# Optimization experiments

Hardware: AMD Instinct MI355X
Metric: run time of the kernel (lower is better)

The kernel has to match this reference:

```python
import jax, jax.numpy as jnp
import numpy as np

SIGNAL_DIM = 64   # D
STATE_DIM = 64    # N
SEQ_LEN = 16384   # L
BATCH = 16


def _init_dplr_hippo(state_dim):
    """NumPy port of init_DPLR_HiPPO(signal_dim=1, state_dim). Returns Lambda,(N,) P,(N,) B,(N,1) complex64."""
    n = np.arange(state_dim, dtype=np.float64)
    A = np.zeros((state_dim, state_dim))
    for k in range(state_dim):
        A[k:, k] = np.sqrt(2.0 * np.arange(k, state_dim) + 1.0) * np.sqrt(2.0 * k + 1.0)
        A[k, k] = k + 1
    A = -A
    P = np.sqrt(n + 0.5)
    SI = A + P[:, None] * P[None, :]
    diag = np.diagonal(SI).copy()
    S = SI - np.diag(diag)
    eigvals, V = np.linalg.eigh(S * -1j)   # S*-1j is Hermitian
    Lam = diag + 1j * eigvals
    Vc = V.conj().T
    Pc = Vc @ P.astype(np.complex128)
    B = np.sqrt(2.0 * n + 1.0)[:, None]    # (N, 1): signal_dim=1, tied across channels
    Bc = Vc @ B.astype(np.complex128)
    return Lam.astype(np.complex64), Pc.astype(np.complex64), Bc.astype(np.complex64)


def _ri(x):
    # complex -> (..., 2) float32, matching torch.view_as_real parameter storage
    return jnp.stack([jnp.real(x), jnp.imag(x)], axis=-1).astype(jnp.float32)


def _to_c(x):
    return jax.lax.complex(x[..., 0], x[..., 1])


def setup_inputs() -> dict:
    key = jax.random.key(0)
    ku, kc1, kc2, kd, ks = jax.random.split(key, 5)
    Lam, P, B = _init_dplr_hippo(STATE_DIM)
    C = (jax.random.normal(kc1, (SIGNAL_DIM, STATE_DIM)) +
         1j * jax.random.normal(kc2, (SIGNAL_DIM, STATE_DIM))).astype(jnp.complex64)
    return {
        "u": jax.random.normal(ku, (BATCH, SEQ_LEN, SIGNAL_DIM), dtype=jnp.float32),
        "Lambda_ri": _ri(jnp.asarray(Lam)),      # (N, 2)
        "P_ri": _ri(jnp.asarray(P)),             # (N, 2)
        "B_ri": _ri(jnp.asarray(B)),             # (N, 1, 2)
        "C_ri": _ri(C),                          # (D, N, 2)
        "D_param": jax.random.normal(kd, (SIGNAL_DIM,), dtype=jnp.float32),
        "log_step": jnp.log(jax.random.uniform(ks, (1,), minval=0.001, maxval=0.1)).astype(jnp.float32),
    }


def reference(u, Lambda_ri, P_ri, B_ri, C_ri, D_param, log_step):
    Lam = _to_c(Lambda_ri)   # (N,)
    P = _to_c(P_ri)          # (N,)
    B = _to_c(B_ri)          # (N, 1)
    C = _to_c(C_ri)          # (D, N)
    L = u.shape[-2]

    step = jnp.exp(log_step)                                  # (1,)
    Omega = jnp.exp(-2j * jnp.pi * (jnp.arange(L) / L))       # (L,) roots of unity
    g = (2.0 / step) * ((1.0 - Omega) / (1.0 + Omega))        # (L,)

    # Batched Cauchy kernel: k_ab[l] = sum_n a_n * b_n / (g_l - Lambda_n)
    cauchy = 1.0 / (g[:, None] - Lam[None, :])                # (L, N)
    a0 = jnp.conj(C)        # (D, N)
    a1 = jnp.conj(P)        # (N,)
    b0 = B[:, 0]            # (N,)  == B.T row (signal_dim=1)
    b1 = P                  # (N,)
    k00 = jnp.einsum('dn,n,ln->dl', a0, b0, cauchy)
    k01 = jnp.einsum('dn,n,ln->dl', a0, b1, cauchy)
    k10 = jnp.einsum('n,n,ln->l', a1, b0, cauchy)
    k11 = jnp.einsum('n,n,ln->l', a1, b1, cauchy)

    evaluated = (2.0 / (1.0 + Omega)) * (k00 - k01 * (1.0 / (1.0 + k11)) * k10)  # (D, L)
    K = jnp.fft.ifft(evaluated, axis=-1).T.real               # (L, D) conv kernel

    # FFT convolution along time axis (zero-pad to 2L, linear convolution)
    ud = jnp.fft.rfft(jnp.pad(u, ((0, 0), (0, L), (0, 0))), axis=-2)
    Kd = jnp.fft.rfft(jnp.pad(K, ((0, L), (0, 0))), axis=-2)
    y = jnp.fft.irfft(ud * Kd, n=2 * L, axis=-2)[..., :L, :]
    return y + D_param * u
```

## Files before the change

kernel.cpp:

```cpp
#include <hip/hip_runtime.h>
#include <math.h>

#define MF 16384
#define HALF 8192

__device__ __forceinline__ float2 cmul(float2 a, float2 b){ return make_float2(a.x*b.x - a.y*b.y, a.x*b.y + a.y*b.x); }
__device__ __forceinline__ float2 cmulc(float2 a, float2 b){ return make_float2(a.x*b.x + a.y*b.y, a.y*b.x - a.x*b.y); }
__device__ __forceinline__ int rho4(int v){ return ((v & 3) << 2) | (v >> 2); }
__device__ __forceinline__ int sob(int k){
    return (rho4(k & 15) << 10) | (rho4((k >> 4) & 15) << 6) | (rho4((k >> 8) & 15) << 2) | (k >> 12);
}
__device__ __forceinline__ int ph(int e){ return e ^ ((e >> 4) & 3) ^ (((e >> 6) & 3) << 2); }

__device__ __forceinline__ void bf4f(float2&a,float2&b,float2&c,float2&d){
    float t0x=a.x+c.x, t0y=a.y+c.y, t2x=a.x-c.x, t2y=a.y-c.y;
    float t1x=b.x+d.x, t1y=b.y+d.y, t3x=b.x-d.x, t3y=b.y-d.y;
    a=make_float2(t0x+t1x,t0y+t1y);
    b=make_float2(t2x+t3y,t2y-t3x);
    c=make_float2(t0x-t1x,t0y-t1y);
    d=make_float2(t2x-t3y,t2y+t3x);
}
__device__ __forceinline__ void bf4i(float2&a,float2&b,float2&c,float2&d){
    float t0x=a.x+c.x, t0y=a.y+c.y, t2x=a.x-c.x, t2y=a.y-c.y;
    float t1x=b.x+d.x, t1y=b.y+d.y, t3x=b.x-d.x, t3y=b.y-d.y;
    a=make_float2(t0x+t1x,t0y+t1y);
    b=make_float2(t2x-t3y,t2y+t3x);
    c=make_float2(t0x-t1x,t0y-t1y);
    d=make_float2(t2x+t3y,t2y-t3x);
}

#define W16_1 make_float2(0.92387953251128674f, -0.38268343236508978f)
#define W16_2 make_float2(0.70710678118654752f, -0.70710678118654752f)
#define W16_3 make_float2(0.38268343236508978f, -0.92387953251128674f)
#define W16_6 make_float2(-0.70710678118654752f, -0.70710678118654752f)
#define W16_9 make_float2(-0.92387953251128674f, 0.38268343236508978f)

__device__ __forceinline__ void dft16_fwd(float2* x){
    bf4f(x[0],x[4],x[8],x[12]);
    bf4f(x[1],x[5],x[9],x[13]);
    bf4f(x[2],x[6],x[10],x[14]);
    bf4f(x[3],x[7],x[11],x[15]);
    x[5]=cmul(x[5],W16_1);  x[9]=cmul(x[9],W16_2);   x[13]=cmul(x[13],W16_3);
    x[6]=cmul(x[6],W16_2);  { float2 t=x[10]; x[10]=make_float2(t.y,-t.x); } x[14]=cmul(x[14],W16_6);
    x[7]=cmul(x[7],W16_3);  x[11]=cmul(x[11],W16_6); x[15]=cmul(x[15],W16_9);
    bf4f(x[0],x[1],x[2],x[3]);
    bf4f(x[4],x[5],x[6],x[7]);
    bf4f(x[8],x[9],x[10],x[11]);
    bf4f(x[12],x[13],x[14],x[15]);
}
__device__ __forceinline__ void dft16_inv(float2* x){
    bf4i(x[0],x[1],x[2],x[3]);
    bf4i(x[4],x[5],x[6],x[7]);
    bf4i(x[8],x[9],x[10],x[11]);
    bf4i(x[12],x[13],x[14],x[15]);
    x[5]=cmulc(x[5],W16_1); x[9]=cmulc(x[9],W16_2);  x[13]=cmulc(x[13],W16_3);
    x[6]=cmulc(x[6],W16_2); { float2 t=x[10]; x[10]=make_float2(-t.y,t.x); } x[14]=cmulc(x[14],W16_6);
    x[7]=cmulc(x[7],W16_3); x[11]=cmulc(x[11],W16_6); x[15]=cmulc(x[15],W16_9);
    bf4i(x[0],x[4],x[8],x[12]);
    bf4i(x[1],x[5],x[9],x[13]);
    bf4i(x[2],x[6],x[10],x[14]);
    bf4i(x[3],x[7],x[11],x[15]);
}

template<bool INV>
__device__ __forceinline__ void pass0(float2* A, const float2* bas, int tid){
    float2 x[16];
    int base = ph(tid);
    #pragma unroll
    for(int m=0;m<16;++m) x[m] = A[base + (m<<10)];
    float2 w1 = bas[tid];
    float2 w2=cmul(w1,w1), w4=cmul(w2,w2), w8=cmul(w4,w4);
    float2 w3=cmul(w2,w1), w5=cmul(w4,w1), w6=cmul(w4,w2), w7=cmul(w4,w3);
    float2 w9=cmul(w8,w1), w10=cmul(w8,w2), w11=cmul(w8,w3), w12=cmul(w8,w4);
    float2 w13=cmul(w8,w5), w14=cmul(w8,w6), w15=cmul(w8,w7);
    if (!INV){
        dft16_fwd(x);
        x[1]=cmul(x[1],w4);   x[2]=cmul(x[2],w8);   x[3]=cmul(x[3],w12);
        x[4]=cmul(x[4],w1);   x[5]=cmul(x[5],w5);   x[6]=cmul(x[6],w9);
        x[7]=cmul(x[7],w13);  x[8]=cmul(x[8],w2);   x[9]=cmul(x[9],w6);
        x[10]=cmul(x[10],w10);x[11]=cmul(x[11],w14);x[12]=cmul(x[12],w3);
        x[13]=cmul(x[13],w7); x[14]=cmul(x[14],w11);x[15]=cmul(x[15],w15);
    } else {
        x[1]=cmulc(x[1],w4);   x[2]=cmulc(x[2],w8);   x[3]=cmulc(x[3],w12);
        x[4]=cmulc(x[4],w1);   x[5]=cmulc(x[5],w5);   x[6]=cmulc(x[6],w9);
        x[7]=cmulc(x[7],w13);  x[8]=cmulc(x[8],w2);   x[9]=cmulc(x[9],w6);
        x[10]=cmulc(x[10],w10);x[11]=cmulc(x[11],w14);x[12]=cmulc(x[12],w3);
        x[13]=cmulc(x[13],w7); x[14]=cmulc(x[14],w11);x[15]=cmulc(x[15],w15);
        dft16_inv(x);
    }
    #pragma unroll
    for(int m=0;m<16;++m) A[base + (m<<10)] = x[m];
}

template<bool INV>
__device__ __forceinline__ void pass1(float2* A, const float2* tw1s, int tid){
    float2 x[16];
    int i1 = tid & 63;
    int B = (tid >> 6) << 10;
    int i1x = i1 ^ ((i1 >> 4) & 3);
    #pragma unroll
    for(int m=0;m<16;++m) x[m] = A[B + (m<<6) + (i1x ^ ((m&3)<<2))];
    if (!INV){
        dft16_fwd(x);
        #pragma unroll
        for(int j=1;j<16;++j) x[j] = cmul(x[j], tw1s[(j<<6)+i1]);
    } else {
        #pragma unroll
        for(int j=1;j<16;++j) x[j] = cmulc(x[j], tw1s[(j<<6)+i1]);
        dft16_inv(x);
    }
    #pragma unroll
    for(int m=0;m<16;++m) A[B + (m<<6) + (i1x ^ ((m&3)<<2))] = x[m];
}

template<bool INV>
__device__ __forceinline__ void pass2(float2* A, const float2* tw2s, int tid){
    float2 x[16];
    int q = tid >> 2, j2 = tid & 3;
    int qb = q << 6;
    int qx = (q & 3) << 2;
    #pragma unroll
    for(int m=0;m<16;++m) x[m] = A[qb + ((((m<<2)|j2) ^ ((m>>2)&3)) ^ qx)];
    if (!INV){
        dft16_fwd(x);
        #pragma unroll
        for(int j=1;j<16;++j) x[j] = cmul(x[j], tw2s[(j<<2)+j2]);
    } else {
        #pragma unroll
        for(int j=1;j<16;++j) x[j] = cmulc(x[j], tw2s[(j<<2)+j2]);
        dft16_inv(x);
    }
    #pragma unroll
    for(int m=0;m<16;++m) A[qb + ((((m<<2)|j2) ^ ((m>>2)&3)) ^ qx)] = x[m];
}

template<bool INV>
__device__ __forceinline__ void pass3(float2* A, int tid){
    int sgm = ((tid>>2)&3) ^ (((tid>>4)&3)<<2);
    #pragma unroll
    for(int rr=0; rr<4; ++rr){
        int base = (tid<<2) | (rr<<12);
        float2 a=A[(base|0)^sgm], b=A[(base|1)^sgm], c=A[(base|2)^sgm], d=A[(base|3)^sgm];
        if(!INV) bf4f(a,b,c,d); else bf4i(a,b,c,d);
        A[(base|0)^sgm]=a; A[(base|1)^sgm]=b; A[(base|2)^sgm]=c; A[(base|3)^sgm]=d;
    }
}

__global__ void k_init(float2* __restrict__ baseg, float2* __restrict__ tw1g, float2* __restrict__ tw2g){
    int id = blockIdx.x * 256 + threadIdx.x;
    const double TP = 6.2831853071795864769;
    if (id < 1024){
        double a = -TP * (double)id / 16384.0;
        baseg[id] = make_float2((float)cos(a), (float)sin(a));
    } else if (id < 2048){
        int q = id - 1024; int j = q >> 6, i1 = q & 63;
        double a = -TP * (double)(i1 * rho4(j)) / 1024.0;
        tw1g[q] = make_float2((float)cos(a), (float)sin(a));
    } else if (id < 2048 + 64){
        int q = id - 2048; int j = q >> 2, i2 = q & 3;
        double a = -TP * (double)(i2 * rho4(j)) / 64.0;
        tw2g[q] = make_float2((float)cos(a), (float)sin(a));
    }
}

__global__ __launch_bounds__(1024) void k_eval(const float2* __restrict__ Lam, const float2* __restrict__ P,
                                               const float2* __restrict__ Bc, const float2* __restrict__ C,
                                               const float* __restrict__ log_step, float2* __restrict__ E) {
    __shared__ float2 bTs[16][64];
    __shared__ float2 pTs[16][64];
    __shared__ float2 S10s[16], S11s[16];
    __shared__ float2 C_l[64][65];
    __shared__ float2 tile[16][65];
    int tid = threadIdx.x;
    int l0 = blockIdx.x * 64;
    float step = expf(log_step[0]);
    {
        int dq = tid >> 6, n = tid & 63;
        #pragma unroll
        for (int p = 0; p < 4; ++p) { int dd = dq + p * 16; C_l[n][dd] = C[dd * 64 + n]; }
    }
    __syncthreads();
    int w = tid >> 6;
    int lane = tid & 63;
    for (int p = 0; p < 4; ++p) {
        int l = l0 + p * 16 + w;
        float lf = (float)l * (1.0f / 16384.0f);
        float s2 = sinpif(lf), c2 = cospif(lf);
        float2 q1 = make_float2(2.0f*c2*c2, -2.0f*s2*c2);
        {
            int n = lane;
            float2 q2 = make_float2(4.0f*s2*s2, 4.0f*s2*c2);
            float2 ln = Lam[n];
            float2 lq = cmul(ln, q1);
            float2 den = make_float2(q2.x - step*lq.x, q2.y - step*lq.y);
            float idn = step / (den.x*den.x + den.y*den.y);
            float2 T = make_float2(den.x*idn, -den.y*idn);
            float2 bn = Bc[n], pn = P[n];
            float2 bT = cmul(bn, T), pT = cmul(pn, T);
            bTs[w][n] = bT; pTs[w][n] = pT;
            float2 s10 = make_float2(pn.x*bT.x + pn.y*bT.y, pn.x*bT.y - pn.y*bT.x);
            float2 s11 = make_float2(pn.x*pT.x + pn.y*pT.y, pn.x*pT.y - pn.y*pT.x);
            #pragma unroll
            for (int off = 32; off > 0; off >>= 1) {
                s10.x += __shfl_xor(s10.x, off);
                s10.y += __shfl_xor(s10.y, off);
                s11.x += __shfl_xor(s11.x, off);
                s11.y += __shfl_xor(s11.y, off);
            }
            if (n == 0) { S10s[w] = s10; S11s[w] = s11; }
        }
        __syncthreads();
        {
            int d = lane;
            float2 S00 = make_float2(0.f, 0.f), S01 = make_float2(0.f, 0.f);
            #pragma unroll 8
            for (int n = 0; n < 64; ++n) {
                float2 cn = C_l[n][d];
                float2 bT = bTs[w][n];
                float2 pT = pTs[w][n];
                S00.x += cn.x*bT.x + cn.y*bT.y;  S00.y += cn.x*bT.y - cn.y*bT.x;
                S01.x += cn.x*pT.x + cn.y*pT.y;  S01.y += cn.x*pT.y - cn.y*pT.x;
            }
            float2 S10 = S10s[w], S11 = S11s[w];
            float2 k11 = cmul(q1, S11); k11.x += 1.0f;
            float2 k10q = cmul(q1, S10);
            float ik = 1.0f / (k11.x*k11.x + k11.y*k11.y);
            float2 quo = make_float2((k10q.x*k11.x + k10q.y*k11.y) * ik,
                                     (k10q.y*k11.x - k10q.x*k11.y) * ik);
            float2 corr = cmul(S01, quo);
            tile[w][d] = make_float2(2.0f*(S00.x - corr.x), 2.0f*(S00.y - corr.y));
        }
        __syncthreads();
        {
            int lo = tid & 15, dq = tid >> 4;
            E[(size_t)dq * MF + l0 + p * 16 + lo] = tile[lo][dq];
        }
        __syncthreads();
    }
}

__global__ __launch_bounds__(1024, 4) void k_prep(const float2* __restrict__ E, float4* __restrict__ Ktab,
                                                  const float2* __restrict__ baseg, const float2* __restrict__ tw1g,
                                                  const float2* __restrict__ tw2g) {
    __shared__ float2 A[MF];
    __shared__ float2 bas[1024];
    __shared__ float2 tw1s[1024];
    __shared__ float2 tw2s[64];
    int d = blockIdx.x, tid = threadIdx.x;
    bas[tid] = baseg[tid];
    tw1s[tid] = tw1g[tid];
    if (tid < 64) tw2s[tid] = tw2g[tid];
    const float2* Ed = E + (size_t)d * MF;
    #pragma unroll
    for (int r = 0; r < 16; ++r) { int l = tid + (r << 10); A[ph(sob(l))] = Ed[l]; }
    __syncthreads();
    pass3<true>(A, tid); __syncthreads();
    pass2<true>(A, tw2s, tid); __syncthreads();
    pass1<true>(A, tw1s, tid); __syncthreads();
    pass0<true>(A, bas, tid); __syncthreads();
    const float s = 1.0f / (float)MF;
    float2 rv[8];
    #pragma unroll
    for (int r = 0; r < 8; ++r) {
        int t = tid + (r << 10);
        rv[r] = make_float2(A[ph(2*t)].x * s, A[ph(2*t+1)].x * s);
    }
    __syncthreads();
    int pht = ph(tid);
    #pragma unroll
    for (int r = 0; r < 16; ++r) A[pht + (r << 10)] = (r < 8) ? rv[r] : make_float2(0.f, 0.f);
    __syncthreads();
    pass0<false>(A, bas, tid); __syncthreads();
    pass1<false>(A, tw1s, tid); __syncthreads();
    pass2<false>(A, tw2s, tid); __syncthreads();
    pass3<false>(A, tid); __syncthreads();
    float4* Kd = Ktab + (size_t)d * MF;
    int Cbits = (rho4(tid >> 6) << 4) | (rho4((tid >> 2) & 15) << 8) | ((tid & 3) << 12);
    const float ksc = 1.0f / (float)MF;
    #pragma unroll
    for (int r = 0; r < 16; ++r) {
        int k = Cbits | rho4(r);
        int kp = (MF - k) & (MF - 1);
        int p = sob(kp);
        float kf = (float)k * (1.0f / 16384.0f);
        float2 w = make_float2(cospif(kf), -sinpif(kf));
        float2 Zk = A[pht + (r << 10)];
        float2 Zm = A[ph(p)]; Zm.y = -Zm.y;
        float2 Ue = make_float2(0.5f*(Zk.x + Zm.x), 0.5f*(Zk.y + Zm.y));
        float2 dd = make_float2(Zk.x - Zm.x, Zk.y - Zm.y);
        float2 Uo = make_float2(0.5f*dd.y, -0.5f*dd.x);
        float2 t2 = cmul(w, Uo);
        Kd[tid + (r << 10)] = make_float4((Ue.x + t2.x)*ksc, (Ue.y + t2.y)*ksc,
                                          (Ue.x - t2.x)*ksc, (Ue.y - t2.y)*ksc);
    }
}

__global__ void k_transpose_in(const float* __restrict__ u, float* __restrict__ uT) {
    __shared__ float tile[64][65];
    int b = blockIdx.y, t0 = blockIdx.x * 64, tid = threadIdx.x;
    #pragma unroll
    for (int k2 = 0; k2 < 16; ++k2) {
        int idx = tid + k2 * 256;
        int tl = idx >> 6, dl = idx & 63;
        tile[tl][dl] = u[((size_t)(b * MF + t0 + tl)) * 64 + dl];
    }
    __syncthreads();
    #pragma unroll
    for (int k2 = 0; k2 < 16; ++k2) {
        int idx = tid + k2 * 256;
        int dl = idx >> 6, tl = idx & 63;
        uT[((size_t)b * 64 + dl) * MF + t0 + tl] = tile[tl][dl];
    }
}

template<bool TRANS>
__global__ __launch_bounds__(1024, 4) void k_conv(const float* __restrict__ u, const float* __restrict__ uT,
                                                  const float4* __restrict__ Ktab, const float* __restrict__ Dp,
                                                  float* __restrict__ yT, float* __restrict__ yout,
                                                  const float2* __restrict__ baseg, const float2* __restrict__ tw1g,
                                                  const float2* __restrict__ tw2g) {
    __shared__ float2 A[MF];
    __shared__ float2 bas[1024];
    __shared__ float2 tw1s[1024];
    __shared__ float2 tw2s[64];
    int tid = threadIdx.x;
    bas[tid] = baseg[tid];
    tw1s[tid] = tw1g[tid];
    if (tid < 64) tw2s[tid] = tw2g[tid];
    int bid = blockIdx.x;
    int vb = ((bid & 7) << 7) | (bid >> 3);
    int d = vb >> 4, b = vb & 15;
    int bd = (b << 6) | d;
    int pht = ph(tid);
    if (TRANS) {
        const float2* src = (const float2*)(uT + (size_t)bd * MF);
        #pragma unroll
        for (int r = 0; r < 16; ++r) {
            int t = tid + (r << 10);
            A[pht + (r << 10)] = (r < 8) ? src[t] : make_float2(0.f, 0.f);
        }
    } else {
        const float* ub = u + ((size_t)b * MF) * 64 + d;
        #pragma unroll
        for (int r = 0; r < 16; ++r) {
            int t = tid + (r << 10);
            float2 v = make_float2(0.f, 0.f);
            if (r < 8) { v.x = ub[(size_t)(2 * t) * 64]; v.y = ub[(size_t)(2 * t + 1) * 64]; }
            A[pht + (r << 10)] = v;
        }
    }
    __syncthreads();
    pass0<false>(A, bas, tid); __syncthreads();
    pass1<false>(A, tw1s, tid); __syncthreads();
    pass2<false>(A, tw2s, tid); __syncthreads();
    const float4* Kd = Ktab + (size_t)d * MF;
    float4 kd[16];
    #pragma unroll
    for (int r = 0; r < 16; ++r) kd[r] = Kd[tid + (r << 10)];
    pass3<false>(A, tid); __syncthreads();
    int Cbits = (rho4(tid >> 6) << 4) | (rho4((tid >> 2) & 15) << 8) | ((tid & 3) << 12);
    float2 Wr[16];
    #pragma unroll
    for (int r = 0; r < 16; ++r) {
        int k = Cbits | rho4(r);
        int kp = (MF - k) & (MF - 1);
        int p = sob(kp);
        float kf = (float)k * (1.0f / 16384.0f);
        float2 w = make_float2(cospif(kf), -sinpif(kf));
        float2 Zk = A[pht + (r << 10)];
        float2 Zm = A[ph(p)]; Zm.y = -Zm.y;
        float2 Ue = make_float2(0.5f*(Zk.x + Zm.x), 0.5f*(Zk.y + Zm.y));
        float2 dd = make_float2(Zk.x - Zm.x, Zk.y - Zm.y);
        float2 Uo = make_float2(0.5f*dd.y, -0.5f*dd.x);
        float2 t2 = cmul(w, Uo);
        float2 X0 = make_float2(Ue.x + t2.x, Ue.y + t2.y);
        float2 X1 = make_float2(Ue.x - t2.x, Ue.y - t2.y);
        float2 Y0 = cmul(X0, make_float2(kd[r].x, kd[r].y));
        float2 Y1 = cmul(X1, make_float2(kd[r].z, kd[r].w));
        float2 Ey = make_float2(0.5f*(Y0.x + Y1.x), 0.5f*(Y0.y + Y1.y));
        float2 Dy = make_float2(Y0.x - Y1.x, Y0.y - Y1.y);
        float2 Oy = cmulc(Dy, w);
        Oy.x *= 0.5f; Oy.y *= 0.5f;
        Wr[r] = make_float2(Ey.x - Oy.y, Ey.y + Oy.x);
    }
    __syncthreads();
    #pragma unroll
    for (int r = 0; r < 16; ++r) A[pht + (r << 10)] = Wr[r];
    __syncthreads();
    pass3<true>(A, tid); __syncthreads();
    pass2<true>(A, tw2s, tid); __syncthreads();
    pass1<true>(A, tw1s, tid); __syncthreads();
    pass0<true>(A, bas, tid); __syncthreads();
    if (TRANS) {
        float2* dst = (float2*)(yT + (size_t)bd * MF);
        #pragma unroll
        for (int r = 0; r < 8; ++r) dst[tid + (r << 10)] = A[pht + (r << 10)];
    } else {
        float Dd = Dp[d];
        float* yb = yout + ((size_t)b * MF) * 64 + d;
        const float* ub = u + ((size_t)b * MF) * 64 + d;
        #pragma unroll
        for (int r = 0; r < 8; ++r) {
            int t = tid + (r << 10);
            float2 v = A[pht + (r << 10)];
            yb[(size_t)(2 * t) * 64]     = v.x + Dd * ub[(size_t)(2 * t) * 64];
            yb[(size_t)(2 * t + 1) * 64] = v.y + Dd * ub[(size_t)(2 * t + 1) * 64];
        }
    }
}

__global__ void k_out(const float* __restrict__ yT, const float* __restrict__ u,
                      const float* __restrict__ Dp, float* __restrict__ y) {
    __shared__ float tile[64][65];
    int b = blockIdx.y, t0 = blockIdx.x * 64, tid = threadIdx.x;
    #pragma unroll
    for (int k2 = 0; k2 < 16; ++k2) {
        int idx = tid + k2 * 256;
        int dl = idx >> 6, tl = idx & 63;
        tile[dl][tl] = yT[((size_t)b * 64 + dl) * MF + t0 + tl];
    }
    __syncthreads();
    #pragma unroll
    for (int k2 = 0; k2 < 16; ++k2) {
        int idx = tid + k2 * 256;
        int tl = idx >> 6, dl = idx & 63;
        size_t gi = ((size_t)(b * MF + t0 + tl)) * 64 + dl;
        y[gi] = tile[dl][tl] + Dp[dl] * u[gi];
    }
}

extern "C" void kernel_launch(void* const* d_in, const int* in_sizes, int n_in,
                              void* d_out, int out_size, void* d_ws, size_t ws_size,
                              hipStream_t stream) {
    const float*  u   = (const float*)d_in[0];
    const float2* Lam = (const float2*)d_in[1];
    const float2* P   = (const float2*)d_in[2];
    const float2* Bc  = (const float2*)d_in[3];
    const float2* C   = (const float2*)d_in[4];
    const float*  Dp  = (const float*)d_in[5];
    const float*  ls  = (const float*)d_in[6];
    float* y = (float*)d_out;
    char* ws = (char*)d_ws;

    size_t off = 0;
    float2* baseg = (float2*)(ws + off); off += (size_t)1024 * sizeof(float2);
    float2* tw1g  = (float2*)(ws + off); off += (size_t)1024 * sizeof(float2);
    float2* tw2g  = (float2*)(ws + off); off += (size_t)64 * sizeof(float2) + 512;
    float2* E     = (float2*)(ws + off); off += (size_t)64 * MF * sizeof(float2);
    float4* Ktab  = (float4*)(ws + off); off += (size_t)64 * MF * sizeof(float4);
    float*  uT    = (float*) (ws + off); off += (size_t)1024 * MF * sizeof(float);
    float*  yT    = (float*) (ws + off); off += (size_t)1024 * MF * sizeof(float);
    bool trans = (ws_size >= off);

    k_init<<<9, 256, 0, stream>>>(baseg, tw1g, tw2g);
    k_eval<<<256, 1024, 0, stream>>>(Lam, P, Bc, C, ls, E);
    k_prep<<<64, 1024, 0, stream>>>(E, Ktab, baseg, tw1g, tw2g);

    if (trans) {
        dim3 tg(MF / 64, 16);
        k_transpose_in<<<tg, 256, 0, stream>>>(u, uT);
        k_conv<true><<<1024, 1024, 0, stream>>>(u, uT, Ktab, Dp, yT, y, baseg, tw1g, tw2g);
        k_out<<<tg, 256, 0, stream>>>(yT, u, Dp, y);
    } else {
        k_conv<false><<<1024, 1024, 0, stream>>>(u, nullptr, Ktab, Dp, nullptr, y, baseg, tw1g, tw2g);
    }
}
```

Measured before the change: 291.1 us.

## Fuse FFT stages, derive twiddles from base table, merge init and transpose launches

Replaces the per-pass twiddle tables with twiddles computed on the fly from a single base root via powers, which cuts shared memory and table loads. The first and last radix-16 passes of the convolution now run straight from and into registers. The final radix-4 pass is fused with the pointwise spectrum multiply into paired quad butterflies that read the kernel table directly. Twiddle init is merged into the eval kernel and the input transpose into the prep kernel, removing two launches, and the D*u skip term moves into the conv epilogue. The cost is more register pressure, more complex pairing logic (with a special case for thread 0), and more work on fewer launches.

```diff
diff --git a/kernel.cpp b/kernel.cpp
--- a/kernel.cpp
+++ b/kernel.cpp
@@ -63,18 +63,12 @@
 }
 
 template<bool INV>
-__device__ __forceinline__ void pass0(float2* A, const float2* bas, int tid){
-    float2 x[16];
-    int base = ph(tid);
-    #pragma unroll
-    for(int m=0;m<16;++m) x[m] = A[base + (m<<10)];
-    float2 w1 = bas[tid];
+__device__ __forceinline__ void tw0_apply(float2* x, float2 w1){
     float2 w2=cmul(w1,w1), w4=cmul(w2,w2), w8=cmul(w4,w4);
     float2 w3=cmul(w2,w1), w5=cmul(w4,w1), w6=cmul(w4,w2), w7=cmul(w4,w3);
     float2 w9=cmul(w8,w1), w10=cmul(w8,w2), w11=cmul(w8,w3), w12=cmul(w8,w4);
     float2 w13=cmul(w8,w5), w14=cmul(w8,w6), w15=cmul(w8,w7);
     if (!INV){
-        dft16_fwd(x);
         x[1]=cmul(x[1],w4);   x[2]=cmul(x[2],w8);   x[3]=cmul(x[3],w12);
         x[4]=cmul(x[4],w1);   x[5]=cmul(x[5],w5);   x[6]=cmul(x[6],w9);
         x[7]=cmul(x[7],w13);  x[8]=cmul(x[8],w2);   x[9]=cmul(x[9],w6);
@@ -86,52 +80,65 @@
         x[7]=cmulc(x[7],w13);  x[8]=cmulc(x[8],w2);   x[9]=cmulc(x[9],w6);
         x[10]=cmulc(x[10],w10);x[11]=cmulc(x[11],w14);x[12]=cmulc(x[12],w3);
         x[13]=cmulc(x[13],w7); x[14]=cmulc(x[14],w11);x[15]=cmulc(x[15],w15);
-        dft16_inv(x);
-    }
+    }
+}
+
+template<bool INV>
+__device__ __forceinline__ void pass0(float2* A, float2 w1g, int tid){
+    float2 x[16];
+    int base = ph(tid);
+    #pragma unroll
+    for(int m=0;m<16;++m) x[m] = A[base + (m<<10)];
+    if(!INV){ dft16_fwd(x); tw0_apply<false>(x, w1g); }
+    else { tw0_apply<true>(x, w1g); dft16_inv(x); }
     #pragma unroll
     for(int m=0;m<16;++m) A[base + (m<<10)] = x[m];
 }
 
 template<bool INV>
-__device__ __forceinline__ void pass1(float2* A, const float2* tw1s, int tid){
+__device__ __forceinline__ void pass1(float2* A, const float2* basP1, int tid){
     float2 x[16];
     int i1 = tid & 63;
     int B = (tid >> 6) << 10;
     int i1x = i1 ^ ((i1 >> 4) & 3);
-    #pragma unroll
-    for(int m=0;m<16;++m) x[m] = A[B + (m<<6) + (i1x ^ ((m&3)<<2))];
-    if (!INV){
-        dft16_fwd(x);
-        #pragma unroll
-        for(int j=1;j<16;++j) x[j] = cmul(x[j], tw1s[(j<<6)+i1]);
-    } else {
-        #pragma unroll
-        for(int j=1;j<16;++j) x[j] = cmulc(x[j], tw1s[(j<<6)+i1]);
-        dft16_inv(x);
-    }
-    #pragma unroll
-    for(int m=0;m<16;++m) A[B + (m<<6) + (i1x ^ ((m&3)<<2))] = x[m];
+    int b0 = B | i1x;
+    int b1 = B | 64 | (i1x ^ 4);
+    int b2 = B | 128 | (i1x ^ 8);
+    int b3 = B | 192 | (i1x ^ 12);
+    x[0]=A[b0];     x[1]=A[b1];     x[2]=A[b2];     x[3]=A[b3];
+    x[4]=A[b0+256]; x[5]=A[b1+256]; x[6]=A[b2+256]; x[7]=A[b3+256];
+    x[8]=A[b0+512]; x[9]=A[b1+512]; x[10]=A[b2+512];x[11]=A[b3+512];
+    x[12]=A[b0+768];x[13]=A[b1+768];x[14]=A[b2+768];x[15]=A[b3+768];
+    float2 w1 = basP1[i1];
+    if(!INV){ dft16_fwd(x); tw0_apply<false>(x, w1); }
+    else { tw0_apply<true>(x, w1); dft16_inv(x); }
+    A[b0]=x[0];     A[b1]=x[1];     A[b2]=x[2];     A[b3]=x[3];
+    A[b0+256]=x[4]; A[b1+256]=x[5]; A[b2+256]=x[6]; A[b3+256]=x[7];
+    A[b0+512]=x[8]; A[b1+512]=x[9]; A[b2+512]=x[10];A[b3+512]=x[11];
+    A[b0+768]=x[12];A[b1+768]=x[13];A[b2+768]=x[14];A[b3+768]=x[15];
 }
 
 template<bool INV>
-__device__ __forceinline__ void pass2(float2* A, const float2* tw2s, int tid){
+__device__ __forceinline__ void pass2(float2* A, const float2* basP2, int tid){
     float2 x[16];
     int q = tid >> 2, j2 = tid & 3;
-    int qb = q << 6;
-    int qx = (q & 3) << 2;
-    #pragma unroll
-    for(int m=0;m<16;++m) x[m] = A[qb + ((((m<<2)|j2) ^ ((m>>2)&3)) ^ qx)];
-    if (!INV){
-        dft16_fwd(x);
-        #pragma unroll
-        for(int j=1;j<16;++j) x[j] = cmul(x[j], tw2s[(j<<2)+j2]);
-    } else {
-        #pragma unroll
-        for(int j=1;j<16;++j) x[j] = cmulc(x[j], tw2s[(j<<2)+j2]);
-        dft16_inv(x);
-    }
-    #pragma unroll
-    for(int m=0;m<16;++m) A[qb + ((((m<<2)|j2) ^ ((m>>2)&3)) ^ qx)] = x[m];
+    int qb = q << 6, qa = q & 3;
+    int c0 = qb | (j2 ^ 0);
+    int c1 = qb | 16 | (j2 ^ 1);
+    int c2 = qb | 32 | (j2 ^ 2);
+    int c3 = qb | 48 | (j2 ^ 3);
+    int r0 = (qa ^ 0) << 2, r1 = (qa ^ 1) << 2, r2 = (qa ^ 2) << 2, r3 = (qa ^ 3) << 2;
+    x[0]=A[c0+r0];  x[1]=A[c0+r1];  x[2]=A[c0+r2];  x[3]=A[c0+r3];
+    x[4]=A[c1+r0];  x[5]=A[c1+r1];  x[6]=A[c1+r2];  x[7]=A[c1+r3];
+    x[8]=A[c2+r0];  x[9]=A[c2+r1];  x[10]=A[c2+r2]; x[11]=A[c2+r3];
+    x[12]=A[c3+r0]; x[13]=A[c3+r1]; x[14]=A[c3+r2]; x[15]=A[c3+r3];
+    float2 w1 = basP2[j2];
+    if(!INV){ dft16_fwd(x); tw0_apply<false>(x, w1); }
+    else { tw0_apply<true>(x, w1); dft16_inv(x); }
+    A[c0+r0]=x[0];  A[c0+r1]=x[1];  A[c0+r2]=x[2];  A[c0+r3]=x[3];
+    A[c1+r0]=x[4];  A[c1+r1]=x[5];  A[c1+r2]=x[6];  A[c1+r3]=x[7];
+    A[c2+r0]=x[8];  A[c2+r1]=x[9];  A[c2+r2]=x[10]; A[c2+r3]=x[11];
+    A[c3+r0]=x[12]; A[c3+r1]=x[13]; A[c3+r2]=x[14]; A[c3+r3]=x[15];
 }
 
 template<bool INV>
@@ -146,32 +153,86 @@
     }
 }
 
-__global__ void k_init(float2* __restrict__ baseg, float2* __restrict__ tw1g, float2* __restrict__ tw2g){
-    int id = blockIdx.x * 256 + threadIdx.x;
-    const double TP = 6.2831853071795864769;
-    if (id < 1024){
-        double a = -TP * (double)id / 16384.0;
-        baseg[id] = make_float2((float)cos(a), (float)sin(a));
-    } else if (id < 2048){
-        int q = id - 1024; int j = q >> 6, i1 = q & 63;
-        double a = -TP * (double)(i1 * rho4(j)) / 1024.0;
-        tw1g[q] = make_float2((float)cos(a), (float)sin(a));
-    } else if (id < 2048 + 64){
-        int q = id - 2048; int j = q >> 2, i2 = q & 3;
-        double a = -TP * (double)(i2 * rho4(j)) / 64.0;
-        tw2g[q] = make_float2((float)cos(a), (float)sin(a));
-    }
-}
-
-__global__ __launch_bounds__(1024) void k_eval(const float2* __restrict__ Lam, const float2* __restrict__ P,
-                                               const float2* __restrict__ Bc, const float2* __restrict__ C,
-                                               const float* __restrict__ log_step, float2* __restrict__ E) {
+__device__ __forceinline__ float2 pw_slot(float2 Zk, float2 Zm, float4 kd, float2 w){
+    Zm.y = -Zm.y;
+    float2 Ue = make_float2(0.5f*(Zk.x+Zm.x), 0.5f*(Zk.y+Zm.y));
+    float2 dd = make_float2(Zk.x-Zm.x, Zk.y-Zm.y);
+    float2 Uo = make_float2(0.5f*dd.y, -0.5f*dd.x);
+    float2 t2 = cmul(w, Uo);
+    float2 X0 = make_float2(Ue.x+t2.x, Ue.y+t2.y);
+    float2 X1 = make_float2(Ue.x-t2.x, Ue.y-t2.y);
+    float2 Y0 = cmul(X0, make_float2(kd.x,kd.y));
+    float2 Y1 = cmul(X1, make_float2(kd.z,kd.w));
+    float2 Ey = make_float2(0.5f*(Y0.x+Y1.x), 0.5f*(Y0.y+Y1.y));
+    float2 Dy = make_float2(Y0.x-Y1.x, Y0.y-Y1.y);
+    float2 Oy = cmulc(Dy, w);
+    return make_float2(Ey.x - 0.5f*Oy.y, Ey.y + 0.5f*Oy.x);
+}
+template<int I>
+__device__ __forceinline__ float2 wslot(float2 wb){
+    const float r2 = 0.70710678118654752f;
+    if (I==0) return wb;
+    if (I==1) return make_float2((wb.x+wb.y)*r2, (wb.y-wb.x)*r2);
+    if (I==2) return make_float2(wb.y, -wb.x);
+    return make_float2((wb.y-wb.x)*r2, -(wb.x+wb.y)*r2);
+}
+__device__ __forceinline__ void quadgeo(int v, int& pb, int& px, int& qs, float2& wb){
+    int qq = rho4((v>>8)&15) | (rho4((v>>4)&15)<<4) | (rho4(v&15)<<8);
+    qs = qq << 2;
+    pb = qs ^ (((qq>>4)&3)<<2);
+    px = (qq>>2)&3;
+    float vf = (float)v * (1.0f/16384.0f);
+    wb = make_float2(cospif(vf), -sinpif(vf));
+}
+template<int MODE>
+__device__ __forceinline__ void pw_pair(float2* A, const float4* Kd,
+        int pba, int pxa, float2 wba, int qsa,
+        int pbb, int pxb, float2 wbb, int qsb){
+    float2 za[4], zb[4];
+    za[0]=A[pba+(0^pxa)]; za[1]=A[pba+(1^pxa)]; za[2]=A[pba+(2^pxa)]; za[3]=A[pba+(3^pxa)];
+    zb[0]=A[pbb+(0^pxb)]; zb[1]=A[pbb+(1^pxb)]; zb[2]=A[pbb+(2^pxb)]; zb[3]=A[pbb+(3^pxb)];
+    bf4f(za[0],za[1],za[2],za[3]);
+    bf4f(zb[0],zb[1],zb[2],zb[3]);
+    float4 ka0=Kd[qsa+0], ka1=Kd[qsa+1], ka2=Kd[qsa+2], ka3=Kd[qsa+3];
+    float4 kb0=Kd[qsb+0], kb1=Kd[qsb+1], kb2=Kd[qsb+2], kb3=Kd[qsb+3];
+    float2 wa[4], wz[4];
+    if (MODE == 0){
+        wa[0]=pw_slot(za[0], zb[3], ka0, wslot<0>(wba));
+        wa[1]=pw_slot(za[1], zb[2], ka1, wslot<1>(wba));
+        wa[2]=pw_slot(za[2], zb[1], ka2, wslot<2>(wba));
+        wa[3]=pw_slot(za[3], zb[0], ka3, wslot<3>(wba));
+        wz[0]=pw_slot(zb[0], za[3], kb0, wslot<0>(wbb));
+        wz[1]=pw_slot(zb[1], za[2], kb1, wslot<1>(wbb));
+        wz[2]=pw_slot(zb[2], za[1], kb2, wslot<2>(wbb));
+        wz[3]=pw_slot(zb[3], za[0], kb3, wslot<3>(wbb));
+    } else {
+        wa[0]=pw_slot(za[0], zb[0], ka0, wslot<0>(wba));
+        wa[1]=pw_slot(za[1], zb[3], ka1, wslot<1>(wba));
+        wa[2]=pw_slot(za[2], zb[2], ka2, wslot<2>(wba));
+        wa[3]=pw_slot(za[3], zb[1], ka3, wslot<3>(wba));
+        wz[0]=wa[0]; wz[1]=wa[1]; wz[2]=wa[2]; wz[3]=wa[3];
+    }
+    bf4i(wa[0],wa[1],wa[2],wa[3]);
+    bf4i(wz[0],wz[1],wz[2],wz[3]);
+    A[pba+(0^pxa)]=wa[0]; A[pba+(1^pxa)]=wa[1]; A[pba+(2^pxa)]=wa[2]; A[pba+(3^pxa)]=wa[3];
+    A[pbb+(0^pxb)]=wz[0]; A[pbb+(1^pxb)]=wz[1]; A[pbb+(2^pxb)]=wz[2]; A[pbb+(3^pxb)]=wz[3];
+}
+
+__global__ __launch_bounds__(1024) void k_evalinit(const float2* __restrict__ Lam, const float2* __restrict__ P,
+        const float2* __restrict__ Bc, const float2* __restrict__ C,
+        const float* __restrict__ log_step, float2* __restrict__ E, float2* __restrict__ baseg) {
     __shared__ float2 bTs[16][64];
     __shared__ float2 pTs[16][64];
     __shared__ float2 S10s[16], S11s[16];
     __shared__ float2 C_l[64][65];
     __shared__ float2 tile[16][65];
     int tid = threadIdx.x;
+    if (blockIdx.x >= 256){
+        const double TP = 6.2831853071795864769;
+        double a = -TP * (double)tid / 16384.0;
+        baseg[tid] = make_float2((float)cos(a), (float)sin(a));
+        return;
+    }
     int l0 = blockIdx.x * 64;
     float step = expf(log_step[0]);
     {
@@ -239,25 +300,48 @@
     }
 }
 
-__global__ __launch_bounds__(1024, 4) void k_prep(const float2* __restrict__ E, float4* __restrict__ Ktab,
-                                                  const float2* __restrict__ baseg, const float2* __restrict__ tw1g,
-                                                  const float2* __restrict__ tw2g) {
-    __shared__ float2 A[MF];
-    __shared__ float2 bas[1024];
-    __shared__ float2 tw1s[1024];
-    __shared__ float2 tw2s[64];
-    int d = blockIdx.x, tid = threadIdx.x;
-    bas[tid] = baseg[tid];
-    tw1s[tid] = tw1g[tid];
-    if (tid < 64) tw2s[tid] = tw2g[tid];
+union MidShm {
+    struct { float2 A[MF]; float2 basP1[64]; float2 basP2[4]; } p;
+    float t[256][65];
+};
+
+__global__ __launch_bounds__(1024, 4) void k_mid(const float2* __restrict__ E, float4* __restrict__ Ktab,
+        const float2* __restrict__ baseg, const float* __restrict__ u, float* __restrict__ uT) {
+    __shared__ MidShm sh;
+    int tid = threadIdx.x;
+    if (blockIdx.x >= 64){
+        int cid = blockIdx.x - 64;
+        int b = cid >> 6, t0c = (cid & 63) << 8;
+        const float* ub = u + ((size_t)(b * MF + t0c)) * 64;
+        #pragma unroll
+        for (int it = 0; it < 16; ++it){
+            int tl = it * 16 + (tid >> 6), dl = tid & 63;
+            sh.t[tl][dl] = ub[(size_t)tl * 64 + dl];
+        }
+        __syncthreads();
+        float* dst = uT + (size_t)b * 64 * MF + t0c;
+        #pragma unroll
+        for (int it = 0; it < 16; ++it){
+            int dd = (tid >> 8) + it * 4, tl = tid & 255;
+            dst[(size_t)dd * MF + tl] = sh.t[tl][dd];
+        }
+        return;
+    }
+    float2* A = sh.p.A;
+    float2* basP1 = sh.p.basP1;
+    float2* basP2 = sh.p.basP2;
+    float2 w1g = baseg[tid];
+    if (tid < 64) basP1[tid] = baseg[tid << 4];
+    if (tid < 4)  basP2[tid] = baseg[tid << 8];
+    int d = blockIdx.x;
     const float2* Ed = E + (size_t)d * MF;
     #pragma unroll
     for (int r = 0; r < 16; ++r) { int l = tid + (r << 10); A[ph(sob(l))] = Ed[l]; }
     __syncthreads();
     pass3<true>(A, tid); __syncthreads();
-    pass2<true>(A, tw2s, tid); __syncthreads();
-    pass1<true>(A, tw1s, tid); __syncthreads();
-    pass0<true>(A, bas, tid); __syncthreads();
+    pass2<true>(A, basP2, tid); __syncthreads();
+    pass1<true>(A, basP1, tid); __syncthreads();
+    pass0<true>(A, w1g, tid); __syncthreads();
     const float s = 1.0f / (float)MF;
     float2 rv[8];
     #pragma unroll
@@ -270,9 +354,9 @@
     #pragma unroll
     for (int r = 0; r < 16; ++r) A[pht + (r << 10)] = (r < 8) ? rv[r] : make_float2(0.f, 0.f);
     __syncthreads();
-    pass0<false>(A, bas, tid); __syncthreads();
-    pass1<false>(A, tw1s, tid); __syncthreads();
-    pass2<false>(A, tw2s, tid); __syncthreads();
+    pass0<false>(A, w1g, tid); __syncthreads();
+    pass1<false>(A, basP1, tid); __syncthreads();
+    pass2<false>(A, basP2, tid); __syncthreads();
     pass3<false>(A, tid); __syncthreads();
     float4* Kd = Ktab + (size_t)d * MF;
     int Cbits = (rho4(tid >> 6) << 4) | (rho4((tid >> 2) & 15) << 8) | ((tid & 3) << 12);
@@ -295,122 +379,88 @@
     }
 }
 
-__global__ void k_transpose_in(const float* __restrict__ u, float* __restrict__ uT) {
-    __shared__ float tile[64][65];
-    int b = blockIdx.y, t0 = blockIdx.x * 64, tid = threadIdx.x;
-    #pragma unroll
-    for (int k2 = 0; k2 < 16; ++k2) {
-        int idx = tid + k2 * 256;
-        int tl = idx >> 6, dl = idx & 63;
-        tile[tl][dl] = u[((size_t)(b * MF + t0 + tl)) * 64 + dl];
-    }
-    __syncthreads();
-    #pragma unroll
-    for (int k2 = 0; k2 < 16; ++k2) {
-        int idx = tid + k2 * 256;
-        int dl = idx >> 6, tl = idx & 63;
-        uT[((size_t)b * 64 + dl) * MF + t0 + tl] = tile[tl][dl];
-    }
-}
-
 template<bool TRANS>
 __global__ __launch_bounds__(1024, 4) void k_conv(const float* __restrict__ u, const float* __restrict__ uT,
-                                                  const float4* __restrict__ Ktab, const float* __restrict__ Dp,
-                                                  float* __restrict__ yT, float* __restrict__ yout,
-                                                  const float2* __restrict__ baseg, const float2* __restrict__ tw1g,
-                                                  const float2* __restrict__ tw2g) {
+        const float4* __restrict__ Ktab, const float* __restrict__ Dp,
+        float* __restrict__ yT, float* __restrict__ yout, const float2* __restrict__ baseg) {
     __shared__ float2 A[MF];
-    __shared__ float2 bas[1024];
-    __shared__ float2 tw1s[1024];
-    __shared__ float2 tw2s[64];
+    __shared__ float2 basP1[64];
+    __shared__ float2 basP2[4];
     int tid = threadIdx.x;
-    bas[tid] = baseg[tid];
-    tw1s[tid] = tw1g[tid];
-    if (tid < 64) tw2s[tid] = tw2g[tid];
+    float2 w1g = baseg[tid];
+    if (tid < 64) basP1[tid] = baseg[tid << 4];
+    if (tid < 4)  basP2[tid] = baseg[tid << 8];
     int bid = blockIdx.x;
     int vb = ((bid & 7) << 7) | (bid >> 3);
     int d = vb >> 4, b = vb & 15;
     int bd = (b << 6) | d;
-    int pht = ph(tid);
-    if (TRANS) {
-        const float2* src = (const float2*)(uT + (size_t)bd * MF);
+    int base = ph(tid);
+    const float2* src = (const float2*)(uT + (size_t)bd * MF);
+    const float* ub = u + ((size_t)b * MF) * 64 + d;
+    {
+        float2 x[16];
         #pragma unroll
-        for (int r = 0; r < 16; ++r) {
-            int t = tid + (r << 10);
-            A[pht + (r << 10)] = (r < 8) ? src[t] : make_float2(0.f, 0.f);
-        }
+        for (int m = 0; m < 16; ++m){
+            if (m < 8){
+                if (TRANS) x[m] = src[tid + (m << 10)];
+                else { int t = tid + (m << 10); x[m] = make_float2(ub[(size_t)(2*t)*64], ub[(size_t)(2*t+1)*64]); }
+            } else x[m] = make_float2(0.f, 0.f);
+        }
+        dft16_fwd(x);
+        tw0_apply<false>(x, w1g);
+        #pragma unroll
+        for (int m = 0; m < 16; ++m) A[base + (m << 10)] = x[m];
+    }
+    __syncthreads();
+    pass1<false>(A, basP1, tid); __syncthreads();
+    pass2<false>(A, basP2, tid); __syncthreads();
+    const float4* Kd = Ktab + (size_t)d * MF;
+    if (tid != 0){
+        int pb0,px0,qs0; float2 wb0; quadgeo(2*tid,      pb0,px0,qs0,wb0);
+        int pb1,px1,qs1; float2 wb1; quadgeo(2*tid+1,    pb1,px1,qs1,wb1);
+        int pb2,px2,qs2; float2 wb2; quadgeo(4096-2*tid, pb2,px2,qs2,wb2);
+        int pb3,px3,qs3; float2 wb3; quadgeo(4095-2*tid, pb3,px3,qs3,wb3);
+        pw_pair<0>(A, Kd, pb0,px0,wb0,qs0, pb2,px2,wb2,qs2);
+        pw_pair<0>(A, Kd, pb1,px1,wb1,qs1, pb3,px3,wb3,qs3);
     } else {
-        const float* ub = u + ((size_t)b * MF) * 64 + d;
+        int pb0,px0,qs0; float2 wb0; quadgeo(0,    pb0,px0,qs0,wb0);
+        int pb1,px1,qs1; float2 wb1; quadgeo(1,    pb1,px1,qs1,wb1);
+        int pb2,px2,qs2; float2 wb2; quadgeo(4095, pb2,px2,qs2,wb2);
+        int pb3,px3,qs3; float2 wb3; quadgeo(2048, pb3,px3,qs3,wb3);
+        pw_pair<1>(A, Kd, pb0,px0,wb0,qs0, pb0,px0,wb0,qs0);
+        pw_pair<0>(A, Kd, pb1,px1,wb1,qs1, pb2,px2,wb2,qs2);
+        pw_pair<0>(A, Kd, pb3,px3,wb3,qs3, pb3,px3,wb3,qs3);
+    }
+    __syncthreads();
+    pass2<true>(A, basP2, tid); __syncthreads();
+    pass1<true>(A, basP1, tid); __syncthreads();
+    {
+        float2 x[16];
         #pragma unroll
-        for (int r = 0; r < 16; ++r) {
-            int t = tid + (r << 10);
-            float2 v = make_float2(0.f, 0.f);
-            if (r < 8) { v.x = ub[(size_t)(2 * t) * 64]; v.y = ub[(size_t)(2 * t + 1) * 64]; }
-            A[pht + (r << 10)] = v;
-        }
-    }
-    __syncthreads();
-    pass0<false>(A, bas, tid); __syncthreads();
-    pass1<false>(A, tw1s, tid); __syncthreads();
-    pass2<false>(A, tw2s, tid); __syncthreads();
-    const float4* Kd = Ktab + (size_t)d * MF;
-    float4 kd[16];
-    #pragma unroll
-    for (int r = 0; r < 16; ++r) kd[r] = Kd[tid + (r << 10)];
-    pass3<false>(A, tid); __syncthreads();
-    int Cbits = (rho4(tid >> 6) << 4) | (rho4((tid >> 2) & 15) << 8) | ((tid & 3) << 12);
-    float2 Wr[16];
-    #pragma unroll
-    for (int r = 0; r < 16; ++r) {
-        int k = Cbits | rho4(r);
-        int kp = (MF - k) & (MF - 1);
-        int p = sob(kp);
-        float kf = (float)k * (1.0f / 16384.0f);
-        float2 w = make_float2(cospif(kf), -sinpif(kf));
-        float2 Zk = A[pht + (r << 10)];
-        float2 Zm = A[ph(p)]; Zm.y = -Zm.y;
-        float2 Ue = make_float2(0.5f*(Zk.x + Zm.x), 0.5f*(Zk.y + Zm.y));
-        float2 dd = make_float2(Zk.x - Zm.x, Zk.y - Zm.y);
-        float2 Uo = make_float2(0.5f*dd.y, -0.5f*dd.x);
-        float2 t2 = cmul(w, Uo);
-        float2 X0 = make_float2(Ue.x + t2.x, Ue.y + t2.y);
-        float2 X1 = make_float2(Ue.x - t2.x, Ue.y - t2.y);
-        float2 Y0 = cmul(X0, make_float2(kd[r].x, kd[r].y));
-        float2 Y1 = cmul(X1, make_float2(kd[r].z, kd[r].w));
-        float2 Ey = make_float2(0.5f*(Y0.x + Y1.x), 0.5f*(Y0.y + Y1.y));
-        float2 Dy = make_float2(Y0.x - Y1.x, Y0.y - Y1.y);
-        float2 Oy = cmulc(Dy, w);
-        Oy.x *= 0.5f; Oy.y *= 0.5f;
-        Wr[r] = make_float2(Ey.x - Oy.y, Ey.y + Oy.x);
-    }
-    __syncthreads();
-    #pragma unroll
-    for (int r = 0; r < 16; ++r) A[pht + (r << 10)] = Wr[r];
-    __syncthreads();
-    pass3<true>(A, tid); __syncthreads();
-    pass2<true>(A, tw2s, tid); __syncthreads();
-    pass1<true>(A, tw1s, tid); __syncthreads();
-    pass0<true>(A, bas, tid); __syncthreads();
-    if (TRANS) {
-        float2* dst = (float2*)(yT + (size_t)bd * MF);
-        #pragma unroll
-        for (int r = 0; r < 8; ++r) dst[tid + (r << 10)] = A[pht + (r << 10)];
-    } else {
+        for (int m = 0; m < 16; ++m) x[m] = A[base + (m << 10)];
+        tw0_apply<true>(x, w1g);
+        dft16_inv(x);
         float Dd = Dp[d];
-        float* yb = yout + ((size_t)b * MF) * 64 + d;
-        const float* ub = u + ((size_t)b * MF) * 64 + d;
-        #pragma unroll
-        for (int r = 0; r < 8; ++r) {
-            int t = tid + (r << 10);
-            float2 v = A[pht + (r << 10)];
-            yb[(size_t)(2 * t) * 64]     = v.x + Dd * ub[(size_t)(2 * t) * 64];
-            yb[(size_t)(2 * t + 1) * 64] = v.y + Dd * ub[(size_t)(2 * t + 1) * 64];
-        }
-    }
-}
-
-__global__ void k_out(const float* __restrict__ yT, const float* __restrict__ u,
-                      const float* __restrict__ Dp, float* __restrict__ y) {
+        if (TRANS){
+            float2* dst = (float2*)(yT + (size_t)bd * MF);
+            #pragma unroll
+            for (int m = 0; m < 8; ++m){
+                float2 s2 = src[tid + (m << 10)];
+                dst[tid + (m << 10)] = make_float2(x[m].x + Dd * s2.x, x[m].y + Dd * s2.y);
+            }
+        } else {
+            float* yb = yout + ((size_t)b * MF) * 64 + d;
+            #pragma unroll
+            for (int m = 0; m < 8; ++m){
+                int t = tid + (m << 10);
+                yb[(size_t)(2*t)*64]   = x[m].x + Dd * ub[(size_t)(2*t)*64];
+                yb[(size_t)(2*t+1)*64] = x[m].y + Dd * ub[(size_t)(2*t+1)*64];
+            }
+        }
+    }
+}
+
+__global__ void k_out(const float* __restrict__ yT, float* __restrict__ y) {
     __shared__ float tile[64][65];
     int b = blockIdx.y, t0 = blockIdx.x * 64, tid = threadIdx.x;
     #pragma unroll
@@ -424,8 +474,7 @@
     for (int k2 = 0; k2 < 16; ++k2) {
         int idx = tid + k2 * 256;
         int tl = idx >> 6, dl = idx & 63;
-        size_t gi = ((size_t)(b * MF + t0 + tl)) * 64 + dl;
-        y[gi] = tile[dl][tl] + Dp[dl] * u[gi];
+        y[((size_t)(b * MF + t0 + tl)) * 64 + dl] = tile[dl][tl];
     }
 }
 
@@ -444,24 +493,19 @@
 
     size_t off = 0;
     float2* baseg = (float2*)(ws + off); off += (size_t)1024 * sizeof(float2);
-    float2* tw1g  = (float2*)(ws + off); off += (size_t)1024 * sizeof(float2);
-    float2* tw2g  = (float2*)(ws + off); off += (size_t)64 * sizeof(float2) + 512;
     float2* E     = (float2*)(ws + off); off += (size_t)64 * MF * sizeof(float2);
     float4* Ktab  = (float4*)(ws + off); off += (size_t)64 * MF * sizeof(float4);
     float*  uT    = (float*) (ws + off); off += (size_t)1024 * MF * sizeof(float);
     float*  yT    = (float*) (ws + off); off += (size_t)1024 * MF * sizeof(float);
     bool trans = (ws_size >= off);
 
-    k_init<<<9, 256, 0, stream>>>(baseg, tw1g, tw2g);
-    k_eval<<<256, 1024, 0, stream>>>(Lam, P, Bc, C, ls, E);
-    k_prep<<<64, 1024, 0, stream>>>(E, Ktab, baseg, tw1g, tw2g);
+    k_evalinit<<<257, 1024, 0, stream>>>(Lam, P, Bc, C, ls, E, baseg);
+    k_mid<<<trans ? 1088 : 64, 1024, 0, stream>>>(E, Ktab, baseg, u, uT);
 
     if (trans) {
-        dim3 tg(MF / 64, 16);
-        k_transpose_in<<<tg, 256, 0, stream>>>(u, uT);
-        k_conv<true><<<1024, 1024, 0, stream>>>(u, uT, Ktab, Dp, yT, y, baseg, tw1g, tw2g);
-        k_out<<<tg, 256, 0, stream>>>(yT, u, Dp, y);
+        k_conv<true><<<1024, 1024, 0, stream>>>(u, uT, Ktab, Dp, yT, y, baseg);
+        k_out<<<dim3(MF / 64, 16), 256, 0, stream>>>(yT, y);
     } else {
-        k_conv<false><<<1024, 1024, 0, stream>>>(u, nullptr, Ktab, Dp, nullptr, y, baseg, tw1g, tw2g);
-    }
-}
+        k_conv<false><<<1024, 1024, 0, stream>>>(u, nullptr, Ktab, Dp, nullptr, y, baseg);
+    }
+}
```

Measured after the change: 306.6 us. 5.3% more time.
